# Performance work log

Hardware: AMD Instinct MI355X
Metric: run time of the kernel (lower is better)

Reference implementation:

```python
import jax, jax.numpy as jnp
import numpy as np

N, F, H, L, E, C = 50000, 256, 64, 8, 1600000, 40
ALPHA, THETA = 0.1, 0.5


def setup_inputs() -> dict:
    key = jax.random.key(0)
    ks = jax.random.split(key, 8)
    x = jax.random.normal(ks[0], (N, F), jnp.float32)
    edge_index = jax.random.randint(ks[1], (2, E), 0, N)
    edge_weight = jax.random.uniform(ks[2], (E,), jnp.float32)
    W0 = jax.random.normal(ks[3], (F, H), jnp.float32) / np.sqrt(F).astype(np.float32)
    b0 = jnp.zeros((H,), jnp.float32)
    Wl = jax.random.normal(ks[4], (L, H, H), jnp.float32) / np.sqrt(H).astype(np.float32)
    W2 = jax.random.normal(ks[5], (H * H, C), jnp.float32) / np.sqrt(H * H).astype(np.float32)
    b2 = jnp.zeros((C,), jnp.float32)
    return dict(x=x, edge_index=edge_index, edge_weight=edge_weight,
                W0=W0, b0=b0, Wl=Wl, W2=W2, b2=b2)


def reference(x, edge_index, edge_weight, W0, b0, Wl, W2, b2):
    src, dst = edge_index[0], edge_index[1]
    # initial projection (dropout p=0.0 is identity)
    h0 = jax.nn.relu(x @ W0 + b0)          # [N, H]
    h = h0
    for l in range(L):
        # GCN2Conv, shared_weights=True, normalize=False
        # SpMM: agg[dst] += w * h[src]
        agg = jax.ops.segment_sum(edge_weight[:, None] * h[src], dst, num_segments=N)
        beta = jnp.float32(np.log(THETA / (l + 1) + 1.0))
        hmix = (1.0 - ALPHA) * agg + ALPHA * h0  # initial residual blend
        h = jax.nn.relu((1.0 - beta) * hmix + beta * (hmix @ Wl[l]))
    # outer-product head: [N,H,H] -> [N, H*H]
    op = jnp.einsum('ni,nj->nij', h, h).reshape(N, H * H)
    logits = op @ W2 + b2                  # [N, C]
    return jax.nn.log_softmax(logits, axis=-1)
```

## Files before the change

kernel.cpp:

```cpp
#include <hip/hip_runtime.h>
#include <hip/hip_bf16.h>
#include <math.h>

#define NN 50000
#define FF 256
#define HH 64
#define LL 8
#define EE 1600000
#define CC 40

#define BK 64
#define NB ((NN + BK - 1) / BK)
#define PBK 4096
#define NPART ((EE + PBK - 1) / PBK)

using short8 = __attribute__((ext_vector_type(8))) short;
using f32x4  = __attribute__((ext_vector_type(4))) float;

static __device__ __forceinline__ unsigned short f2b(float f) {
    union { __hip_bfloat16 h; unsigned short u; } cv;
    cv.h = __float2bfloat16(f);
    return cv.u;
}
static __device__ __forceinline__ float b2f(unsigned short u) {
    return __uint_as_float((unsigned)u << 16);
}


__global__ void k_hist(const int* __restrict__ dst, int* __restrict__ cnt) {
    int e = blockIdx.x * 256 + threadIdx.x;
    if (e < EE) atomicAdd(&cnt[dst[e]], 1);
}

__global__ void k_scanA(const int* __restrict__ cnt, int* __restrict__ incl, int* __restrict__ bsum) {
    __shared__ int buf[1024];
    int i = blockIdx.x * 1024 + threadIdx.x;
    int v = (i < NN) ? cnt[i] : 0;
    buf[threadIdx.x] = v;
    __syncthreads();
    for (int off = 1; off < 1024; off <<= 1) {
        int t = (threadIdx.x >= off) ? buf[threadIdx.x - off] : 0;
        __syncthreads();
        buf[threadIdx.x] += t;
        __syncthreads();
    }
    if (i < NN) incl[i] = buf[threadIdx.x];
    if (threadIdx.x == 1023) bsum[blockIdx.x] = buf[1023];
}

__global__ void k_scanB(int* __restrict__ bsum) {
    int t = threadIdx.x;
    int vin = (t < 49) ? bsum[t] : 0;
    int v = vin;
    for (int off = 1; off < 64; off <<= 1) {
        int u = __shfl_up(v, off);
        if (t >= off) v += u;
    }
    if (t < 49) bsum[t] = v - vin;
}

__global__ void k_scanC(const int* __restrict__ cnt, const int* __restrict__ incl,
                        const int* __restrict__ bsum, int* __restrict__ row_ptr) {
    int i = blockIdx.x * 1024 + threadIdx.x;
    if (i < NN) row_ptr[i] = incl[i] - cnt[i] + bsum[blockIdx.x];
    if (i == 0) row_ptr[NN] = EE;
}

__global__ void k_binit(const int* __restrict__ row_ptr, int* __restrict__ bcur) {
    int t = blockIdx.x * 256 + threadIdx.x;
    if (t < NB) bcur[t] = row_ptr[t * BK];
}

__global__ void k_part(const int* __restrict__ src, const int* __restrict__ dst,
                       const float* __restrict__ w, int* __restrict__ bcur,
                       uint2* __restrict__ ebuk) {
    __shared__ int lh[NB];
    __shared__ int lbase[NB];
    int t = threadIdx.x;
    int e0 = blockIdx.x * PBK;
    int e1 = min(e0 + PBK, EE);
    for (int i = t; i < NB; i += 256) lh[i] = 0;
    __syncthreads();
    for (int e = e0 + t; e < e1; e += 256)
        atomicAdd(&lh[(unsigned)dst[e] >> 6], 1);
    __syncthreads();
    for (int i = t; i < NB; i += 256) {
        int c = lh[i];
        lbase[i] = c ? atomicAdd(&bcur[i], c) : 0;
    }
    __syncthreads();
    for (int i = t; i < NB; i += 256) lh[i] = 0;
    __syncthreads();
    for (int e = e0 + t; e < e1; e += 256) {
        int d = dst[e];
        int b = (unsigned)d >> 6;
        int r = atomicAdd(&lh[b], 1);
        ebuk[lbase[b] + r] = make_uint2(((unsigned)src[e] << 16) | (unsigned)f2b(w[e]),
                                        (unsigned)d);
    }
}

__global__ void k_sub(const int* __restrict__ row_ptr, const uint2* __restrict__ ebuk,
                      unsigned* __restrict__ pay) {
    __shared__ int lcur[BK];
    int b = blockIdx.x;
    int d0 = b * BK;
    int t = threadIdx.x;
    if (t < BK && d0 + t < NN) lcur[t] = row_ptr[d0 + t];
    __syncthreads();
    int lo = row_ptr[d0];
    int hi = row_ptr[min(d0 + BK, NN)];
    for (int i = lo + t; i < hi; i += 256) {
        uint2 pk = ebuk[i];
        int p = atomicAdd(&lcur[pk.y - d0], 1);
        pay[p] = pk.x;
    }
}

__global__ __launch_bounds__(512) void k_h0m(const float* __restrict__ x,
                                             const float* __restrict__ W0,
                                             const float* __restrict__ b0,
                                             float* __restrict__ h0f,
                                             unsigned short* __restrict__ h0b) {
    __shared__ __align__(16) __hip_bfloat16 ax[256][72];
    __shared__ __align__(16) __hip_bfloat16 bw[64][72];

    int tid = threadIdx.x;
    int lane = tid & 63;
    int w = tid >> 6;
    int nbase = blockIdx.x * 256;

    f32x4 acc[2][4];
#pragma unroll
    for (int nf = 0; nf < 2; ++nf)
#pragma unroll
        for (int cf = 0; cf < 4; ++cf) acc[nf][cf] = (f32x4){0.f, 0.f, 0.f, 0.f};

    int arow = w * 32 + (lane & 15);
    int kq = (lane >> 4) * 8;

    for (int kc = 0; kc < 4; ++kc) {
        __syncthreads();
#pragma unroll
        for (int p = 0; p < 8; ++p) {
            int q = p * 512 + tid;
            int r = q >> 4, cq = q & 15;
            int node = nbase + r;
            float4 v = {0.f, 0.f, 0.f, 0.f};
            if (node < NN) v = *(const float4*)&x[(size_t)node * FF + kc * 64 + cq * 4];
            __hip_bfloat16* d = &ax[r][cq * 4];
            d[0] = __float2bfloat16(v.x);
            d[1] = __float2bfloat16(v.y);
            d[2] = __float2bfloat16(v.z);
            d[3] = __float2bfloat16(v.w);
        }
#pragma unroll
        for (int u = 0; u < 8; ++u) {
            int k = (tid >> 6) * 8 + u;
            float v = W0[(size_t)(kc * 64 + k) * HH + lane];
            bw[lane][k] = __float2bfloat16(v);
        }
        __syncthreads();
#pragma unroll
        for (int ks = 0; ks < 2; ++ks) {
            short8 a0 = *(const short8*)&ax[arow][ks * 32 + kq];
            short8 a1 = *(const short8*)&ax[arow + 16][ks * 32 + kq];
#pragma unroll
            for (int cf = 0; cf < 4; ++cf) {
                short8 b = *(const short8*)&bw[cf * 16 + (lane & 15)][ks * 32 + kq];
                acc[0][cf] = __builtin_amdgcn_mfma_f32_16x16x32_bf16(a0, b, acc[0][cf], 0, 0, 0);
                acc[1][cf] = __builtin_amdgcn_mfma_f32_16x16x32_bf16(a1, b, acc[1][cf], 0, 0, 0);
            }
        }
    }

#pragma unroll
    for (int nf = 0; nf < 2; ++nf) {
#pragma unroll
        for (int cf = 0; cf < 4; ++cf) {
            int c = cf * 16 + (lane & 15);
            float bias = b0[c];
#pragma unroll
            for (int r = 0; r < 4; ++r) {
                int node = nbase + w * 32 + nf * 16 + ((lane >> 4) << 2) + r;
                if (node < NN) {
                    float v = fmaxf(acc[nf][cf][r] + bias, 0.f);
                    h0f[(size_t)node * HH + c] = v;
                    h0b[(size_t)node * HH + c] = f2b(v);
                }
            }
        }
    }
}

__global__ __launch_bounds__(256, 8) void k_layer(
        const unsigned short* __restrict__ hin, const float* __restrict__ h0,
        const int* __restrict__ row_ptr, const unsigned* __restrict__ pay,
        const float* __restrict__ Wl, float beta,
        unsigned short* __restrict__ hout) {
    int lane = threadIdx.x & 63;
    int half = lane >> 5;
    int j = lane & 31;
    int n0 = (blockIdx.x * 4 + (threadIdx.x >> 6)) * 4;

    const unsigned* __restrict__ hin32 = (const unsigned*)hin;

    float hmix[4];
#pragma unroll
    for (int u = 0; u < 4; ++u) {
        int n = n0 + u;
        int rb = row_ptr[n], re = row_ptr[n + 1];
        float ax0 = 0.f, ay0 = 0.f, ax1 = 0.f, ay1 = 0.f;
        for (int base = rb; base < re; base += 64) {
            int idx = base + lane;
            unsigned pv = (idx < re) ? pay[idx] : 0u;
            int ecnt = min(64, re - base);
            for (int k = 0; k < ecnt; k += 8) {
                unsigned pk[8];
#pragma unroll
                for (int t = 0; t < 8; t++)
                    pk[t] = (unsigned)__builtin_amdgcn_readlane((int)pv, k + t);
                unsigned m0 = half ? pk[1] : pk[0];
                unsigned m1 = half ? pk[3] : pk[2];
                unsigned m2 = half ? pk[5] : pk[4];
                unsigned m3 = half ? pk[7] : pk[6];
                unsigned u0 = hin32[(size_t)(m0 >> 16) * 32 + j];
                unsigned u1 = hin32[(size_t)(m1 >> 16) * 32 + j];
                unsigned u2 = hin32[(size_t)(m2 >> 16) * 32 + j];
                unsigned u3 = hin32[(size_t)(m3 >> 16) * 32 + j];
                float w0 = __uint_as_float((m0 & 0xFFFFu) << 16);
                float w1 = __uint_as_float((m1 & 0xFFFFu) << 16);
                float w2 = __uint_as_float((m2 & 0xFFFFu) << 16);
                float w3 = __uint_as_float((m3 & 0xFFFFu) << 16);
                ax0 = fmaf(w0, __uint_as_float(u0 << 16), ax0);
                ay0 = fmaf(w0, __uint_as_float(u0 & 0xFFFF0000u), ay0);
                ax1 = fmaf(w1, __uint_as_float(u1 << 16), ax1);
                ay1 = fmaf(w1, __uint_as_float(u1 & 0xFFFF0000u), ay1);
                ax0 = fmaf(w2, __uint_as_float(u2 << 16), ax0);
                ay0 = fmaf(w2, __uint_as_float(u2 & 0xFFFF0000u), ay0);
                ax1 = fmaf(w3, __uint_as_float(u3 << 16), ax1);
                ay1 = fmaf(w3, __uint_as_float(u3 & 0xFFFF0000u), ay1);
            }
        }
        float ax = ax0 + ax1, ay = ay0 + ay1;
        ax += __shfl_xor(ax, 32);
        ay += __shfl_xor(ay, 32);
        float vx = __shfl(ax, lane >> 1);
        float vy = __shfl(ay, lane >> 1);
        float acc = (lane & 1) ? vy : vx;
        hmix[u] = fmaf(0.9f, acc, 0.1f * h0[(size_t)n * HH + lane]);
    }

    int hb[4];
#pragma unroll
    for (int u = 0; u < 4; ++u) hb[u] = __float_as_int(hmix[u]);
    float a2[4] = {0.f, 0.f, 0.f, 0.f};
#pragma unroll
    for (int jj = 0; jj < HH; jj++) {
        float wr = Wl[jj * HH + lane];
#pragma unroll
        for (int u = 0; u < 4; ++u) {
            float hj = __int_as_float(__builtin_amdgcn_readlane(hb[u], jj));
            a2[u] = fmaf(hj, wr, a2[u]);
        }
    }
#pragma unroll
    for (int u = 0; u < 4; ++u) {
        float outv = (1.f - beta) * hmix[u] + beta * a2[u];
        hout[(size_t)(n0 + u) * HH + lane] = f2b(fmaxf(outv, 0.f));
    }
}

__global__ __launch_bounds__(512) void k_head(const unsigned short* __restrict__ h,
                                              const float* __restrict__ W2,
                                              const float* __restrict__ b2,
                                              float* __restrict__ out) {
    __shared__ __align__(16) unsigned short hb[256][72];
    __shared__ float hf[256][65];
    __shared__ __align__(16) __hip_bfloat16 Bc[8][48][72];

    int tid = threadIdx.x;
    int lane = tid & 63;
    int w = tid >> 6;
    int nbase = blockIdx.x * 256;

#pragma unroll
    for (int p = 0; p < 32; ++p) {
        int idx = p * 512 + tid;
        int r = idx >> 6, c = idx & 63;
        int node = nbase + r;
        unsigned short raw = (node < NN) ? h[(size_t)node * HH + c] : 0;
        hf[r][c] = b2f(raw);
        hb[r][c] = raw;
    }
    for (int p = tid; p < 8 * 8 * 64; p += 512) {
        int il = p >> 9;
        int c = 40 + ((p >> 6) & 7);
        int jx = p & 63;
        Bc[il][c][jx] = __float2bfloat16(0.f);
    }

    f32x4 acc[2][3];
#pragma unroll
    for (int nf = 0; nf < 2; ++nf)
#pragma unroll
        for (int ct = 0; ct < 3; ++ct) acc[nf][ct] = (f32x4){0.f, 0.f, 0.f, 0.f};

    const f32x4 zf = (f32x4){0.f, 0.f, 0.f, 0.f};
    int arow0 = w * 32 + (lane & 15);
    int kq = (lane >> 4) * 8;
    int rb4 = w * 32 + ((lane >> 4) << 2);

    for (int ic = 0; ic < 8; ++ic) {
        __syncthreads();
#pragma unroll
        for (int p = 0; p < 10; ++p) {
            int q = p * 512 + tid;
            int cq = q % 10;
            int jj = (q / 10) & 63;
            int il = q / 640;
            const float4 v = *(const float4*)&W2[(((size_t)(ic * 8 + il) * 64 + jj) * CC) + cq * 4];
            Bc[il][cq * 4 + 0][jj] = __float2bfloat16(v.x);
            Bc[il][cq * 4 + 1][jj] = __float2bfloat16(v.y);
            Bc[il][cq * 4 + 2][jj] = __float2bfloat16(v.z);
            Bc[il][cq * 4 + 3][jj] = __float2bfloat16(v.w);
        }
        __syncthreads();

#pragma unroll
        for (int il = 0; il < 8; ++il) {
            int ii = ic * 8 + il;
            short8 a0k0 = *(const short8*)&hb[arow0][kq];
            short8 a0k1 = *(const short8*)&hb[arow0][32 + kq];
            short8 a1k0 = *(const short8*)&hb[arow0 + 16][kq];
            short8 a1k1 = *(const short8*)&hb[arow0 + 16][32 + kq];
            short8 b0k0 = *(const short8*)&Bc[il][(lane & 15)][kq];
            short8 b0k1 = *(const short8*)&Bc[il][(lane & 15)][32 + kq];
            short8 b1k0 = *(const short8*)&Bc[il][16 + (lane & 15)][kq];
            short8 b1k1 = *(const short8*)&Bc[il][16 + (lane & 15)][32 + kq];
            short8 b2k0 = *(const short8*)&Bc[il][32 + (lane & 15)][kq];
            short8 b2k1 = *(const short8*)&Bc[il][32 + (lane & 15)][32 + kq];
            float s0[4], s1[4];
#pragma unroll
            for (int r = 0; r < 4; ++r) {
                s0[r] = hf[rb4 + r][ii];
                s1[r] = hf[rb4 + 16 + r][ii];
            }
            f32x4 t;
            t = __builtin_amdgcn_mfma_f32_16x16x32_bf16(a0k0, b0k0, zf, 0, 0, 0);
            t = __builtin_amdgcn_mfma_f32_16x16x32_bf16(a0k1, b0k1, t, 0, 0, 0);
#pragma unroll
            for (int r = 0; r < 4; ++r) acc[0][0][r] = fmaf(s0[r], t[r], acc[0][0][r]);
            t = __builtin_amdgcn_mfma_f32_16x16x32_bf16(a0k0, b1k0, zf, 0, 0, 0);
            t = __builtin_amdgcn_mfma_f32_16x16x32_bf16(a0k1, b1k1, t, 0, 0, 0);
#pragma unroll
            for (int r = 0; r < 4; ++r) acc[0][1][r] = fmaf(s0[r], t[r], acc[0][1][r]);
            t = __builtin_amdgcn_mfma_f32_16x16x32_bf16(a0k0, b2k0, zf, 0, 0, 0);
            t = __builtin_amdgcn_mfma_f32_16x16x32_bf16(a0k1, b2k1, t, 0, 0, 0);
#pragma unroll
            for (int r = 0; r < 4; ++r) acc[0][2][r] = fmaf(s0[r], t[r], acc[0][2][r]);
            t = __builtin_amdgcn_mfma_f32_16x16x32_bf16(a1k0, b0k0, zf, 0, 0, 0);
            t = __builtin_amdgcn_mfma_f32_16x16x32_bf16(a1k1, b0k1, t, 0, 0, 0);
#pragma unroll
            for (int r = 0; r < 4; ++r) acc[1][0][r] = fmaf(s1[r], t[r], acc[1][0][r]);
            t = __builtin_amdgcn_mfma_f32_16x16x32_bf16(a1k0, b1k0, zf, 0, 0, 0);
            t = __builtin_amdgcn_mfma_f32_16x16x32_bf16(a1k1, b1k1, t, 0, 0, 0);
#pragma unroll
            for (int r = 0; r < 4; ++r) acc[1][1][r] = fmaf(s1[r], t[r], acc[1][1][r]);
            t = __builtin_amdgcn_mfma_f32_16x16x32_bf16(a1k0, b2k0, zf, 0, 0, 0);
            t = __builtin_amdgcn_mfma_f32_16x16x32_bf16(a1k1, b2k1, t, 0, 0, 0);
#pragma unroll
            for (int r = 0; r < 4; ++r) acc[1][2][r] = fmaf(s1[r], t[r], acc[1][2][r]);
        }
    }

#pragma unroll
    for (int nf = 0; nf < 2; ++nf) {
#pragma unroll
        for (int ct = 0; ct < 3; ++ct) {
            int c = ct * 16 + (lane & 15);
            if (c < CC) {
                float bias = b2[c];
#pragma unroll
                for (int r = 0; r < 4; ++r) {
                    int node = nbase + w * 32 + nf * 16 + ((lane >> 4) << 2) + r;
                    if (node < NN) out[(size_t)node * CC + c] = acc[nf][ct][r] + bias;
                }
            }
        }
    }
}

__global__ void k_lsm(float* __restrict__ out) {
    int lane = threadIdx.x & 63;
    int n = (blockIdx.x * 256 + threadIdx.x) >> 6;
    if (n >= NN) return;
    float x = (lane < CC) ? out[(size_t)n * CC + lane] : -INFINITY;
    float m = x;
    for (int off = 32; off; off >>= 1) m = fmaxf(m, __shfl_xor(m, off));
    float e = (lane < CC) ? expf(x - m) : 0.f;
    float s = e;
    for (int off = 32; off; off >>= 1) s += __shfl_xor(s, off);
    float lse = m + logf(s);
    if (lane < CC) out[(size_t)n * CC + lane] = x - lse;
}

extern "C" void kernel_launch(void* const* d_in, const int* in_sizes, int n_in,
                              void* d_out, int out_size, void* d_ws, size_t ws_size,
                              hipStream_t stream) {
    const float* x  = (const float*)d_in[0];
    const int*   ei = (const int*)d_in[1];
    const float* ew = (const float*)d_in[2];
    const float* W0 = (const float*)d_in[3];
    const float* b0 = (const float*)d_in[4];
    const float* Wl = (const float*)d_in[5];
    const float* W2 = (const float*)d_in[6];
    const float* b2 = (const float*)d_in[7];
    float* out = (float*)d_out;

    char* ws = (char*)d_ws;
    size_t off = 0;
    auto alloc = [&](size_t b) { size_t o = off; off += (b + 255) & ~(size_t)255; return o; };
    float*          h0f = (float*)(ws + alloc((size_t)NN * HH * 4));
    unsigned short* h0b = (unsigned short*)(ws + alloc((size_t)NN * HH * 2));
    unsigned short* hA  = (unsigned short*)(ws + alloc((size_t)NN * HH * 2));
    unsigned short* hB  = (unsigned short*)(ws + alloc((size_t)NN * HH * 2));
    int*      cnt     = (int*)(ws + alloc((size_t)NN * 4));
    int*      incl    = (int*)(ws + alloc((size_t)NN * 4));
    int*      bsum    = (int*)(ws + alloc(256));
    int*      row_ptr = (int*)(ws + alloc((size_t)(NN + 1) * 4));
    int*      bcur    = (int*)(ws + alloc((size_t)NB * 4));
    uint2*    ebuk    = (uint2*)(ws + alloc((size_t)EE * 8));
    unsigned* pay     = (unsigned*)(ws + alloc((size_t)EE * 4));

    const int* srcp = ei;
    const int* dstp = ei + EE;

    hipMemsetAsync(cnt, 0, (size_t)NN * 4, stream);
    k_hist<<<(EE + 255) / 256, 256, 0, stream>>>(dstp, cnt);
    k_scanA<<<49, 1024, 0, stream>>>(cnt, incl, bsum);
    k_scanB<<<1, 64, 0, stream>>>(bsum);
    k_scanC<<<49, 1024, 0, stream>>>(cnt, incl, bsum, row_ptr);
    k_binit<<<(NB + 255) / 256, 256, 0, stream>>>(row_ptr, bcur);
    k_part<<<NPART, 256, 0, stream>>>(srcp, dstp, ew, bcur, ebuk);
    k_sub<<<NB, 256, 0, stream>>>(row_ptr, ebuk, pay);

    k_h0m<<<196, 512, 0, stream>>>(x, W0, b0, h0f, h0b);

    const unsigned short* hin = h0b;
    unsigned short* ho = hA;
    for (int l = 0; l < LL; l++) {
        float beta = (float)log(0.5 / (double)(l + 1) + 1.0);
        k_layer<<<3125, 256, 0, stream>>>(hin, h0f, row_ptr, pay,
                                          Wl + (size_t)l * HH * HH, beta, ho);
        hin = ho;
        ho = (ho == hA) ? hB : hA;
    }

    k_head<<<196, 512, 0, stream>>>(hin, W2, b2, out);
    k_lsm<<<(NN * 64 + 255) / 256, 256, 0, stream>>>(out);
}
```

Measured before the change: 550.9 us.

## Split head kernel across class tiles and hoist A fragments to registers

The output-head kernel now launches a 2D grid with one block per 16-class tile, so each block loads and converts only its slice of W2. The A fragments from h are loaded once into registers instead of on every inner iteration. The per-row scale values come from the bf16 h buffer as vector loads, which removes the separate fp32 shared copy. This triples the block count (196 to 588) for better occupancy and smaller shared memory, at the cost of each block reloading the h tile and the MFMA A work being repeated across the three class tiles.

```diff
diff --git a/kernel.cpp b/kernel.cpp
--- a/kernel.cpp
+++ b/kernel.cpp
@@ -276,117 +276,89 @@
                                               const float* __restrict__ b2,
                                               float* __restrict__ out) {
     __shared__ __align__(16) unsigned short hb[256][72];
-    __shared__ float hf[256][65];
-    __shared__ __align__(16) __hip_bfloat16 Bc[8][48][72];
+    __shared__ __align__(16) unsigned short Bc[8][16][72];
 
     int tid = threadIdx.x;
     int lane = tid & 63;
     int w = tid >> 6;
     int nbase = blockIdx.x * 256;
+    int ct = blockIdx.y;
+    int c0 = ct * 16;
 
 #pragma unroll
     for (int p = 0; p < 32; ++p) {
         int idx = p * 512 + tid;
         int r = idx >> 6, c = idx & 63;
         int node = nbase + r;
-        unsigned short raw = (node < NN) ? h[(size_t)node * HH + c] : 0;
-        hf[r][c] = b2f(raw);
-        hb[r][c] = raw;
-    }
-    for (int p = tid; p < 8 * 8 * 64; p += 512) {
-        int il = p >> 9;
-        int c = 40 + ((p >> 6) & 7);
-        int jx = p & 63;
-        Bc[il][c][jx] = __float2bfloat16(0.f);
-    }
-
-    f32x4 acc[2][3];
-#pragma unroll
-    for (int nf = 0; nf < 2; ++nf)
-#pragma unroll
-        for (int ct = 0; ct < 3; ++ct) acc[nf][ct] = (f32x4){0.f, 0.f, 0.f, 0.f};
+        hb[r][c] = (node < NN) ? h[(size_t)node * HH + c] : 0;
+    }
+    __syncthreads();
+
+    int kq = (lane >> 4) * 8;
+    int arow = w * 32 + (lane & 15);
+    int rb4 = w * 32 + ((lane >> 4) << 2);
+
+    short8 af00 = *(const short8*)&hb[arow][kq];
+    short8 af01 = *(const short8*)&hb[arow][32 + kq];
+    short8 af10 = *(const short8*)&hb[arow + 16][kq];
+    short8 af11 = *(const short8*)&hb[arow + 16][32 + kq];
 
     const f32x4 zf = (f32x4){0.f, 0.f, 0.f, 0.f};
-    int arow0 = w * 32 + (lane & 15);
-    int kq = (lane >> 4) * 8;
-    int rb4 = w * 32 + ((lane >> 4) << 2);
+    f32x4 acc0 = zf, acc1 = zf;
 
     for (int ic = 0; ic < 8; ++ic) {
         __syncthreads();
 #pragma unroll
-        for (int p = 0; p < 10; ++p) {
+        for (int p = 0; p < 4; ++p) {
             int q = p * 512 + tid;
-            int cq = q % 10;
-            int jj = (q / 10) & 63;
-            int il = q / 640;
-            const float4 v = *(const float4*)&W2[(((size_t)(ic * 8 + il) * 64 + jj) * CC) + cq * 4];
-            Bc[il][cq * 4 + 0][jj] = __float2bfloat16(v.x);
-            Bc[il][cq * 4 + 1][jj] = __float2bfloat16(v.y);
-            Bc[il][cq * 4 + 2][jj] = __float2bfloat16(v.z);
-            Bc[il][cq * 4 + 3][jj] = __float2bfloat16(v.w);
-        }
-        __syncthreads();
+            int cq = q & 3;
+            int jj = (q >> 2) & 63;
+            int il = q >> 8;
+            int c4 = c0 + cq * 4;
+            float4 v = {0.f, 0.f, 0.f, 0.f};
+            if (c4 < CC)
+                v = *(const float4*)&W2[((size_t)(ic * 8 + il) * 64 + jj) * CC + c4];
+            Bc[il][cq * 4 + 0][jj] = f2b(v.x);
+            Bc[il][cq * 4 + 1][jj] = f2b(v.y);
+            Bc[il][cq * 4 + 2][jj] = f2b(v.z);
+            Bc[il][cq * 4 + 3][jj] = f2b(v.w);
+        }
+        __syncthreads();
+
+        short8 sreg[8];
+#pragma unroll
+        for (int r = 0; r < 4; ++r) {
+            sreg[r]     = *(const short8*)&hb[rb4 + r][ic * 8];
+            sreg[4 + r] = *(const short8*)&hb[rb4 + 16 + r][ic * 8];
+        }
 
 #pragma unroll
         for (int il = 0; il < 8; ++il) {
-            int ii = ic * 8 + il;
-            short8 a0k0 = *(const short8*)&hb[arow0][kq];
-            short8 a0k1 = *(const short8*)&hb[arow0][32 + kq];
-            short8 a1k0 = *(const short8*)&hb[arow0 + 16][kq];
-            short8 a1k1 = *(const short8*)&hb[arow0 + 16][32 + kq];
-            short8 b0k0 = *(const short8*)&Bc[il][(lane & 15)][kq];
-            short8 b0k1 = *(const short8*)&Bc[il][(lane & 15)][32 + kq];
-            short8 b1k0 = *(const short8*)&Bc[il][16 + (lane & 15)][kq];
-            short8 b1k1 = *(const short8*)&Bc[il][16 + (lane & 15)][32 + kq];
-            short8 b2k0 = *(const short8*)&Bc[il][32 + (lane & 15)][kq];
-            short8 b2k1 = *(const short8*)&Bc[il][32 + (lane & 15)][32 + kq];
-            float s0[4], s1[4];
-#pragma unroll
-            for (int r = 0; r < 4; ++r) {
-                s0[r] = hf[rb4 + r][ii];
-                s1[r] = hf[rb4 + 16 + r][ii];
-            }
+            short8 b0 = *(const short8*)&Bc[il][lane & 15][kq];
+            short8 b1 = *(const short8*)&Bc[il][lane & 15][32 + kq];
             f32x4 t;
-            t = __builtin_amdgcn_mfma_f32_16x16x32_bf16(a0k0, b0k0, zf, 0, 0, 0);
-            t = __builtin_amdgcn_mfma_f32_16x16x32_bf16(a0k1, b0k1, t, 0, 0, 0);
-#pragma unroll
-            for (int r = 0; r < 4; ++r) acc[0][0][r] = fmaf(s0[r], t[r], acc[0][0][r]);
-            t = __builtin_amdgcn_mfma_f32_16x16x32_bf16(a0k0, b1k0, zf, 0, 0, 0);
-            t = __builtin_amdgcn_mfma_f32_16x16x32_bf16(a0k1, b1k1, t, 0, 0, 0);
-#pragma unroll
-            for (int r = 0; r < 4; ++r) acc[0][1][r] = fmaf(s0[r], t[r], acc[0][1][r]);
-            t = __builtin_amdgcn_mfma_f32_16x16x32_bf16(a0k0, b2k0, zf, 0, 0, 0);
-            t = __builtin_amdgcn_mfma_f32_16x16x32_bf16(a0k1, b2k1, t, 0, 0, 0);
-#pragma unroll
-            for (int r = 0; r < 4; ++r) acc[0][2][r] = fmaf(s0[r], t[r], acc[0][2][r]);
-            t = __builtin_amdgcn_mfma_f32_16x16x32_bf16(a1k0, b0k0, zf, 0, 0, 0);
-            t = __builtin_amdgcn_mfma_f32_16x16x32_bf16(a1k1, b0k1, t, 0, 0, 0);
-#pragma unroll
-            for (int r = 0; r < 4; ++r) acc[1][0][r] = fmaf(s1[r], t[r], acc[1][0][r]);
-            t = __builtin_amdgcn_mfma_f32_16x16x32_bf16(a1k0, b1k0, zf, 0, 0, 0);
-            t = __builtin_amdgcn_mfma_f32_16x16x32_bf16(a1k1, b1k1, t, 0, 0, 0);
-#pragma unroll
-            for (int r = 0; r < 4; ++r) acc[1][1][r] = fmaf(s1[r], t[r], acc[1][1][r]);
-            t = __builtin_amdgcn_mfma_f32_16x16x32_bf16(a1k0, b2k0, zf, 0, 0, 0);
-            t = __builtin_amdgcn_mfma_f32_16x16x32_bf16(a1k1, b2k1, t, 0, 0, 0);
-#pragma unroll
-            for (int r = 0; r < 4; ++r) acc[1][2][r] = fmaf(s1[r], t[r], acc[1][2][r]);
-        }
-    }
-
-#pragma unroll
-    for (int nf = 0; nf < 2; ++nf) {
-#pragma unroll
-        for (int ct = 0; ct < 3; ++ct) {
-            int c = ct * 16 + (lane & 15);
-            if (c < CC) {
-                float bias = b2[c];
-#pragma unroll
-                for (int r = 0; r < 4; ++r) {
-                    int node = nbase + w * 32 + nf * 16 + ((lane >> 4) << 2) + r;
-                    if (node < NN) out[(size_t)node * CC + c] = acc[nf][ct][r] + bias;
-                }
-            }
+            t = __builtin_amdgcn_mfma_f32_16x16x32_bf16(af00, b0, zf, 0, 0, 0);
+            t = __builtin_amdgcn_mfma_f32_16x16x32_bf16(af01, b1, t, 0, 0, 0);
+#pragma unroll
+            for (int r = 0; r < 4; ++r)
+                acc0[r] = fmaf(b2f((unsigned short)sreg[r][il]), t[r], acc0[r]);
+            t = __builtin_amdgcn_mfma_f32_16x16x32_bf16(af10, b0, zf, 0, 0, 0);
+            t = __builtin_amdgcn_mfma_f32_16x16x32_bf16(af11, b1, t, 0, 0, 0);
+#pragma unroll
+            for (int r = 0; r < 4; ++r)
+                acc1[r] = fmaf(b2f((unsigned short)sreg[4 + r][il]), t[r], acc1[r]);
+        }
+    }
+
+    int c = c0 + (lane & 15);
+    if (c < CC) {
+        float bias = b2[c];
+#pragma unroll
+        for (int r = 0; r < 4; ++r) {
+            int node0 = nbase + rb4 + r;
+            if (node0 < NN) out[(size_t)node0 * CC + c] = acc0[r] + bias;
+            int node1 = nbase + rb4 + 16 + r;
+            if (node1 < NN) out[(size_t)node1 * CC + c] = acc1[r] + bias;
         }
     }
 }
@@ -457,6 +429,6 @@
         ho = (ho == hA) ? hB : hA;
     }
 
-    k_head<<<196, 512, 0, stream>>>(hin, W2, b2, out);
+    k_head<<<dim3(196, 3), 512, 0, stream>>>(hin, W2, b2, out);
     k_lsm<<<(NN * 64 + 255) / 256, 256, 0, stream>>>(out);
 }
```

New measurement: 556.9 us. Within noise of the previous version (+1.1%).
